# Kernel tuning notes

Measured on AMD Instinct MI355X. Metric: run time of the kernel, lower is better.

## Reference

```python
import jax, jax.numpy as jnp
import numpy as np

B, N, D, H, NC = 4, 32, 128, 8, 27
DK = D // H
DFF = 4 * D
L = NC * N


def layer_norm(x, g, b, eps=1e-5):
    mu = jnp.mean(x, -1, keepdims=True)
    var = jnp.var(x, -1, keepdims=True)
    return (x - mu) * jax.lax.rsqrt(var + eps) * g + b


def setup_inputs() -> dict:
    ks = jax.random.split(jax.random.key(0), 16)
    s = 1.0 / np.sqrt(D)
    return {
        'x': jax.random.normal(ks[0], (B, N, D), jnp.float32),
        'mask': jax.random.randint(ks[1], (B, 1, N), 0, 2, jnp.int32),
        'coords': jax.random.normal(ks[2], (B, NC, N, 3), jnp.float32),
        'Wp': jax.random.normal(ks[3], (3, D), jnp.float32) * 0.5,
        'bp': jnp.zeros((D,), jnp.float32),
        'Wq': jax.random.normal(ks[4], (D, D), jnp.float32) * s,
        'bq': jnp.zeros((D,), jnp.float32),
        'Wk': jax.random.normal(ks[5], (D, D), jnp.float32) * s,
        'bk': jnp.zeros((D,), jnp.float32),
        'Wv': jax.random.normal(ks[6], (D, D), jnp.float32) * s,
        'bv': jnp.zeros((D,), jnp.float32),
        'Wo': jax.random.normal(ks[7], (D, D), jnp.float32) * s,
        'bo': jnp.zeros((D,), jnp.float32),
        'g1': jnp.ones((D,), jnp.float32),
        'b1': jnp.zeros((D,), jnp.float32),
        'g2': jnp.ones((D,), jnp.float32),
        'b2': jnp.zeros((D,), jnp.float32),
        'W1': jax.random.normal(ks[8], (D, DFF), jnp.float32) * s,
        'bf1': jnp.zeros((DFF,), jnp.float32),
        'W2': jax.random.normal(ks[9], (DFF, D), jnp.float32) * (1.0 / np.sqrt(DFF)),
        'bf2': jnp.zeros((D,), jnp.float32),
    }


def reference(x, mask, coords, Wp, bp, Wq, bq, Wk, bk, Wv, bv, Wo, bo,
              g1, b1, g2, b2, W1, bf1, W2, bf2):
    mask_enh = jnp.tile(mask, (1, NC, 1)).reshape(B, 1, 1, L)

    def step(i):
        # position_encoding: x broadcast over 27 images + linear of coords relative to atom i
        ci = jax.lax.dynamic_slice_in_dim(coords, i, 1, axis=2)        # [B,NC,1,3]
        ar = x[:, None] + (coords - ci) @ Wp + bp                      # [B,NC,N,D]
        a = ar.reshape(B, L, D)
        hn = layer_norm(a, g1, b1)
        q = (hn @ Wq + bq).reshape(B, L, H, DK).transpose(0, 2, 1, 3)
        k = (hn @ Wk + bk).reshape(B, L, H, DK).transpose(0, 2, 1, 3)
        v = (hn @ Wv + bv).reshape(B, L, H, DK).transpose(0, 2, 1, 3)
        scores = jnp.einsum('bhqd,bhkd->bhqk', q, k) / np.sqrt(DK)     # [B,H,L,L]
        scores = jnp.where(mask_enh == 0, -1e9, scores)
        att = jnp.einsum('bhqk,bhkd->bhqd', jax.nn.softmax(scores, -1), v)
        att = att.transpose(0, 2, 1, 3).reshape(B, L, D) @ Wo + bo
        s = a + att  # SublayerConnection (dropout identity in eval)
        # original keeps only [b, image 0, atom i] of the [B,NC,N,D] reshape; flat index = i
        return jax.lax.dynamic_slice_in_dim(s, i, 1, axis=1)[:, 0]     # [B,D]

    rows = jax.lax.map(step, jnp.arange(N))                            # [N,B,D]
    y = rows.transpose(1, 0, 2)                                        # [B,N,D]
    hn2 = layer_norm(y, g2, b2)
    return y + (jax.nn.relu(hn2 @ W1 + bf1) @ W2 + bf2)
```

## Files before the change

### kernel.cpp

```cpp
#include <hip/hip_runtime.h>


#define B_ 4
#define N_ 32
#define D_ 128
#define H_ 8
#define NC_ 27
#define DFF_ 512
#define L_ (NC_*N_)

__device__ __forceinline__ float wred(float v){
  #pragma unroll
  for (int off = 32; off; off >>= 1) v += __shfl_xor(v, off);
  return v;
}

__global__ __launch_bounds__(1024) void k_fused(
    const float* __restrict__ x, const int* __restrict__ mask,
    const float* __restrict__ coords,
    const float* __restrict__ Wp, const float* __restrict__ bp,
    const float* __restrict__ Wq, const float* __restrict__ bq,
    const float* __restrict__ Wk, const float* __restrict__ bk,
    const float* __restrict__ Wv, const float* __restrict__ bv,
    const float* __restrict__ Wo, const float* __restrict__ bo,
    const float* __restrict__ g1, const float* __restrict__ b1,
    const float* __restrict__ g2, const float* __restrict__ b2,
    const float* __restrict__ W1, const float* __restrict__ bf1,
    const float* __restrict__ W2, const float* __restrict__ bfb2,
    float* __restrict__ out)
{
  __shared__ float is_s[L_];
  __shared__ float dc_s[3][L_];
  __shared__ float xg_s[N_][D_+1];
  __shared__ float zz_s[H_][D_+1];
  __shared__ float w_s[3][D_];
  __shared__ float wcg_s[3][D_];
  __shared__ float g1_s[D_], b1_s[D_], bp_s[D_], bq_s[D_], bk_s[D_];
  __shared__ float g2_s[D_], b2_s[D_], bv_s[D_], bo_s[D_], bfb2_s[D_];
  __shared__ float bf1_s[DFF_];
  __shared__ float q_s[D_], hn_s[D_], hn2_s[D_], att_s[D_], y_s[D_];
  __shared__ float qAxk_s[H_][N_];
  __shared__ float qGk_s[H_][3];
  __shared__ float S3_s[H_];
  __shared__ float varx_s[N_];
  __shared__ float dxp_s[N_][3];
  __shared__ int   mask_s[N_];
  __shared__ float cq_s[NC_][3];
  __shared__ float mwp_s[3], P6_s[6];
  __shared__ float pmax_s[H_][2];
  __shared__ float Tnp_s[H_][2][N_];
  __shared__ float Sp_s[H_][2], RDp_s[H_][2][3];
  __shared__ float f_s[DFF_];
  __shared__ float pf_s[4096];
  float4* pf4 = (float4*)pf_s;

  int bi = blockIdx.x;
  int b = bi >> 5, i = bi & 31;
  int tid = threadIdx.x, wave = tid >> 6, lane = tid & 63;
  int es = tid >> 5, d4 = tid & 31;
  int e0 = 2*lane, e1 = 2*lane+1;

  int r0 = wave*2, r1 = wave*2+1;
  float2 xA = *(const float2*)&x[(size_t)(b*N_+r0)*D_ + e0];
  float2 xB = *(const float2*)&x[(size_t)(b*N_+r1)*D_ + e0];
  float2 xI = {0.f, 0.f};
  if (wave == 0) xI = *(const float2*)&x[(size_t)bi*D_ + e0];
  float ck0=0.f, ck1=0.f, ck2=0.f;
  if (tid < L_){
    int c = tid >> 5, n = tid & 31;
    const float* ck = coords + ((size_t)(b*NC_+c)*N_ + n)*3;
    ck0 = ck[0]; ck1 = ck[1]; ck2 = ck[2];
  }
  float4 wq4[4];
  #pragma unroll
  for (int k=0;k<4;k++)
    wq4[k] = *(const float4*)(Wq + (size_t)(es*4+k)*D_ + d4*4);
  float4 wk4[4];
  {
    int h = tid>>7, e = tid&127;
    #pragma unroll
    for (int k=0;k<4;k++)
      wk4[k] = *(const float4*)(Wk + (size_t)e*D_ + h*16 + k*4);
  }
  if (tid < 384) w_s[tid>>7][tid&127] = Wp[tid];
  if      (tid < 128)  g1_s[tid]      = g1[tid];
  else if (tid < 256)  b1_s[tid-128]  = b1[tid-128];
  else if (tid < 384)  bp_s[tid-256]  = bp[tid-256];
  else if (tid < 512)  bq_s[tid-384]  = bq[tid-384];
  else if (tid < 640)  bk_s[tid-512]  = bk[tid-512];
  else if (tid < 768)  g2_s[tid-640]  = g2[tid-640];
  else if (tid < 896)  b2_s[tid-768]  = b2[tid-768];
  else                 bv_s[tid-896]  = bv[tid-896];
  if      (tid < 128)  bo_s[tid]      = bo[tid];
  else if (tid < 256)  bfb2_s[tid-128]= bfb2[tid-128];
  else if (tid < 768)  bf1_s[tid-256] = bf1[tid-256];
  else if (tid < 800)  mask_s[tid-768]= mask[b*N_ + (tid-768)];
  else if (tid < 881){
    int t = tid-800;
    cq_s[t/3][t%3] = coords[((size_t)(b*NC_ + t/3)*N_ + i)*3 + t%3];
  }
  __syncthreads();

  {
    float t0 = xA.x + bp_s[e0], t1 = xA.y + bp_s[e1];
    float mean = wred(t0+t1)*(1.f/D_);
    float h0 = t0-mean, h1 = t1-mean;
    xg_s[r0][e0] = h0*g1_s[e0];
    xg_s[r0][e1] = h1*g1_s[e1];
    float vv = h0*h0 + h1*h1;
    float d0 = h0*w_s[0][e0] + h1*w_s[0][e1];
    float d1 = h0*w_s[1][e0] + h1*w_s[1][e1];
    float d2 = h0*w_s[2][e0] + h1*w_s[2][e1];
    #pragma unroll
    for (int off=32; off; off>>=1){
      vv += __shfl_xor(vv,off); d0 += __shfl_xor(d0,off);
      d1 += __shfl_xor(d1,off); d2 += __shfl_xor(d2,off);
    }
    if (lane==0){ varx_s[r0]=vv*(1.f/D_);
      dxp_s[r0][0]=d0; dxp_s[r0][1]=d1; dxp_s[r0][2]=d2; }
    t0 = xB.x + bp_s[e0]; t1 = xB.y + bp_s[e1];
    mean = wred(t0+t1)*(1.f/D_);
    h0 = t0-mean; h1 = t1-mean;
    xg_s[r1][e0] = h0*g1_s[e0];
    xg_s[r1][e1] = h1*g1_s[e1];
    vv = h0*h0 + h1*h1;
    d0 = h0*w_s[0][e0] + h1*w_s[0][e1];
    d1 = h0*w_s[1][e0] + h1*w_s[1][e1];
    d2 = h0*w_s[2][e0] + h1*w_s[2][e1];
    #pragma unroll
    for (int off=32; off; off>>=1){
      vv += __shfl_xor(vv,off); d0 += __shfl_xor(d0,off);
      d1 += __shfl_xor(d1,off); d2 += __shfl_xor(d2,off);
    }
    if (lane==0){ varx_s[r1]=vv*(1.f/D_);
      dxp_s[r1][0]=d0; dxp_s[r1][1]=d1; dxp_s[r1][2]=d2; }
  }
  float dc0=0.f, dc1=0.f, dc2=0.f;
  if (tid < L_){
    int c = tid >> 5;
    dc0 = ck0 - cq_s[c][0]; dc1 = ck1 - cq_s[c][1]; dc2 = ck2 - cq_s[c][2];
    dc_s[0][tid]=dc0; dc_s[1][tid]=dc1; dc_s[2][tid]=dc2;
  }
  if (wave >= 8 && wave < 11){
    int j = wave - 8;
    float s = w_s[j][lane] + w_s[j][lane+64];
    s = wred(s);
    if (lane==0) mwp_s[j] = s*(1.f/D_);
  }
  if (wave >= 10){
    int idx = wave - 10;
    int ja = (idx>=3) + (idx>=5);
    int jb = idx - (idx>=3)*2 - (idx>=5);
    float s = w_s[ja][lane]*w_s[jb][lane] + w_s[ja][lane+64]*w_s[jb][lane+64];
    s = wred(s);
    if (lane==0) P6_s[idx] = s;
  }
  __syncthreads();

  if (tid < L_){
    int n = tid & 31;
    float m0 = mwp_s[0], m1 = mwp_s[1], m2 = mwp_s[2];
    float M00 = P6_s[0]-D_*m0*m0, M01 = P6_s[1]-D_*m0*m1;
    float M02 = P6_s[2]-D_*m0*m2, M11 = P6_s[3]-D_*m1*m1;
    float M12 = P6_s[4]-D_*m1*m2, M22 = P6_s[5]-D_*m2*m2;
    float quad = dc0*dc0*M00 + dc1*dc1*M11 + dc2*dc2*M22
               + 2.f*(dc0*dc1*M01 + dc0*dc2*M02 + dc1*dc2*M12);
    float lin  = dc0*dxp_s[n][0] + dc1*dxp_s[n][1] + dc2*dxp_s[n][2];
    float E = varx_s[n] + (quad + 2.f*lin)*(1.f/D_);
    is_s[tid] = rsqrtf(fmaxf(E, 0.f) + 1e-5f);
  }
  if (tid < 384){ int j=tid>>7, e=tid&127;
    wcg_s[j][e] = (w_s[j][e] - mwp_s[j])*g1_s[e]; }
  if (tid >= 896){ int e = tid-896;
    hn_s[e] = xg_s[i][e]*rsqrtf(varx_s[i]+1e-5f) + b1_s[e]; }
  __syncthreads();

  {
    float4 acc = {0.f,0.f,0.f,0.f};
    #pragma unroll
    for (int k=0;k<4;k++){
      float h = hn_s[es*4+k];
      acc.x += h*wq4[k].x; acc.y += h*wq4[k].y;
      acc.z += h*wq4[k].z; acc.w += h*wq4[k].w;
    }
    pf4[es*32 + d4] = acc;
  }
  __syncthreads();

  if (tid < D_){
    float a = bq_s[tid];
    #pragma unroll
    for (int s=0;s<32;s++) a += pf_s[s*D_+tid];
    q_s[tid] = a;
  }
  __syncthreads();

  {
    int h = tid>>7, e = tid&127;
    float s = 0.f;
    #pragma unroll
    for (int kq=0; kq<4; kq++){
      s += wk4[kq].x*q_s[h*16+kq*4+0] + wk4[kq].y*q_s[h*16+kq*4+1]
         + wk4[kq].z*q_s[h*16+kq*4+2] + wk4[kq].w*q_s[h*16+kq*4+3];
    }
    zz_s[h][e] = s;
  }
  __syncthreads();

  {
    int quarter = tid>>8, id = tid&255, h = id>>5, n = id&31;
    float s = 0.f;
    #pragma unroll 8
    for (int e = quarter*32; e < quarter*32+32; e++) s += xg_s[n][e]*zz_s[h][e];
    pf_s[quarter*256 + id] = s;
  }
  __syncthreads();

  if (tid < 256){
    qAxk_s[tid>>5][tid&31] = pf_s[tid] + pf_s[256+tid]
                           + pf_s[512+tid] + pf_s[768+tid];
  }
  if (wave >= 8){
    int h = wave - 8;
    float u0 = zz_s[h][lane], u1 = zz_s[h][lane+64];
    float s3 = b1_s[lane]*u0 + b1_s[lane+64]*u1;
    if (lane < 16) s3 += q_s[h*16+lane]*bk_s[h*16+lane];
    float qg0 = wcg_s[0][lane]*u0 + wcg_s[0][lane+64]*u1;
    float qg1 = wcg_s[1][lane]*u0 + wcg_s[1][lane+64]*u1;
    float qg2 = wcg_s[2][lane]*u0 + wcg_s[2][lane+64]*u1;
    #pragma unroll
    for (int off=32; off; off>>=1){
      s3  += __shfl_xor(s3,off);  qg0 += __shfl_xor(qg0,off);
      qg1 += __shfl_xor(qg1,off); qg2 += __shfl_xor(qg2,off);
    }
    if (lane==0){ S3_s[h]=s3; qGk_s[h][0]=qg0; qGk_s[h][1]=qg1; qGk_s[h][2]=qg2; }
  }
  __syncthreads();

  int h2 = wave>>1, sub = wave&1, n2 = lane&31, half2 = lane>>5;
  int q4 = sub*2 + half2, c0 = q4*7, c1 = (q4==3) ? NC_ : c0+7;
  float sc[7];
  {
    float qa = qAxk_s[h2][n2];
    float qg0 = qGk_s[h2][0], qg1 = qGk_s[h2][1], qg2 = qGk_s[h2][2];
    float s3 = S3_s[h2];
    bool mk = mask_s[n2] != 0;
    float M = -3.0e38f;
    #pragma unroll
    for (int t=0; t<7; t++){
      int c = c0+t;
      if (c < c1){
        int l = c*N_ + n2;
        float v = 0.25f*(is_s[l]*(qa + dc_s[0][l]*qg0 + dc_s[1][l]*qg1
                                     + dc_s[2][l]*qg2) + s3);
        sc[t] = mk ? v : -1e9f;
      } else sc[t] = -3.0e38f;
      M = fmaxf(M, sc[t]);
    }
    #pragma unroll
    for (int off=32; off; off>>=1) M = fmaxf(M, __shfl_xor(M, off));
    if (lane==0) pmax_s[h2][sub] = M;
  }
  __syncthreads();

  float4 wv4[4];
  #pragma unroll
  for (int k=0;k<4;k++)
    wv4[k] = *(const float4*)(Wv + (size_t)(es*4+k)*D_ + d4*4);
  {
    float M = fmaxf(pmax_s[h2][0], pmax_s[h2][1]);
    float S=0.f, Tn=0.f, rr0=0.f, rr1=0.f, rr2=0.f;
    #pragma unroll
    for (int t=0; t<7; t++){
      int c = c0+t;
      if (c < c1){
        int l = c*N_ + n2;
        float w_ = __expf(sc[t] - M);
        float tt = w_ * is_s[l];
        S += w_; Tn += tt;
        rr0 += tt*dc_s[0][l]; rr1 += tt*dc_s[1][l]; rr2 += tt*dc_s[2][l];
      }
    }
    float Tn2 = Tn + __shfl_xor(Tn, 32);
    if (lane < 32) Tnp_s[h2][sub][lane] = Tn2;
    #pragma unroll
    for (int off=32; off; off>>=1){
      S   += __shfl_xor(S,off);   rr0 += __shfl_xor(rr0,off);
      rr1 += __shfl_xor(rr1,off); rr2 += __shfl_xor(rr2,off);
    }
    if (lane==0){ Sp_s[h2][sub]=S;
      RDp_s[h2][sub][0]=rr0; RDp_s[h2][sub][1]=rr1; RDp_s[h2][sub][2]=rr2; }
  }
  __syncthreads();

  float4 wo4[4];
  #pragma unroll
  for (int k=0;k<4;k++)
    wo4[k] = *(const float4*)(Wo + (size_t)(es*4+k)*D_ + d4*4);
  {
    int h = tid>>7, e = tid&127;
    float rS = 1.f / fmaxf(Sp_s[h][0]+Sp_s[h][1], 1e-30f);
    float z = 0.f;
    #pragma unroll 8
    for (int n=0; n<N_; n++){
      float Tn = Tnp_s[h][0][n] + Tnp_s[h][1][n];
      z += Tn * xg_s[n][e];
    }
    float R0 = RDp_s[h][0][0]+RDp_s[h][1][0];
    float R1 = RDp_s[h][0][1]+RDp_s[h][1][1];
    float R2 = RDp_s[h][0][2]+RDp_s[h][1][2];
    z += R0*wcg_s[0][e] + R1*wcg_s[1][e] + R2*wcg_s[2][e];
    zz_s[h][e] = z*rS + b1_s[e];
  }
  __syncthreads();

  {
    int h = d4 >> 2;
    float4 acc = {0.f,0.f,0.f,0.f};
    #pragma unroll
    for (int k=0;k<4;k++){
      float zv = zz_s[h][es*4+k];
      acc.x += zv*wv4[k].x; acc.y += zv*wv4[k].y;
      acc.z += zv*wv4[k].z; acc.w += zv*wv4[k].w;
    }
    pf4[es*32 + d4] = acc;
  }
  __syncthreads();

  if (tid < D_){
    float a = bv_s[tid];
    #pragma unroll
    for (int s=0;s<32;s++) a += pf_s[s*D_+tid];
    att_s[tid] = a;
  }
  __syncthreads();

  int e8 = tid>>7, c4 = tid&127;
  float4 w1a[8];
  #pragma unroll
  for (int k=0;k<8;k++)
    w1a[k] = *(const float4*)(W1 + (size_t)(e8*16+k)*DFF_ + c4*4);
  {
    float4 acc = {0.f,0.f,0.f,0.f};
    #pragma unroll
    for (int k=0;k<4;k++){
      float av = att_s[es*4+k];
      acc.x += av*wo4[k].x; acc.y += av*wo4[k].y;
      acc.z += av*wo4[k].z; acc.w += av*wo4[k].w;
    }
    pf4[es*32 + d4] = acc;
  }
  __syncthreads();

  if (wave == 0){
    float y0 = xI.x + bp_s[e0] + bo_s[e0];
    float y1 = xI.y + bp_s[e1] + bo_s[e1];
    #pragma unroll
    for (int s=0;s<32;s++){
      float2 p = *(const float2*)&pf_s[s*D_ + e0];
      y0 += p.x; y1 += p.y;
    }
    y_s[e0] = y0; y_s[e1] = y1;
    float mean = wred(y0+y1)*(1.f/D_);
    float v0 = y0-mean, v1 = y1-mean;
    float var = wred(v0*v0+v1*v1)*(1.f/D_);
    float isd = rsqrtf(var + 1e-5f);
    hn2_s[e0] = v0*isd*g2_s[e0] + b2_s[e0];
    hn2_s[e1] = v1*isd*g2_s[e1] + b2_s[e1];
  }
  __syncthreads();

  int js = tid>>5;
  float4 w2a[8];
  {
    float4 w1b[8];
    #pragma unroll
    for (int k=0;k<8;k++)
      w1b[k] = *(const float4*)(W1 + (size_t)(e8*16+8+k)*DFF_ + c4*4);
    float4 acc = {0.f,0.f,0.f,0.f};
    #pragma unroll
    for (int k=0;k<8;k++){
      float h = hn2_s[e8*16+k];
      acc.x += h*w1a[k].x; acc.y += h*w1a[k].y;
      acc.z += h*w1a[k].z; acc.w += h*w1a[k].w;
    }
    #pragma unroll
    for (int k=0;k<8;k++){
      float h = hn2_s[e8*16+8+k];
      acc.x += h*w1b[k].x; acc.y += h*w1b[k].y;
      acc.z += h*w1b[k].z; acc.w += h*w1b[k].w;
    }
    #pragma unroll
    for (int k=0;k<8;k++)
      w2a[k] = *(const float4*)(W2 + (size_t)(js*16+k)*D_ + d4*4);
    pf4[e8*128 + c4] = acc;
  }
  __syncthreads();

  if (tid < DFF_){
    float a = bf1_s[tid];
    #pragma unroll
    for (int s=0;s<8;s++) a += pf_s[s*DFF_+tid];
    f_s[tid] = fmaxf(a, 0.f);
  }
  __syncthreads();

  {
    float4 w2b[8];
    #pragma unroll
    for (int k=0;k<8;k++)
      w2b[k] = *(const float4*)(W2 + (size_t)(js*16+8+k)*D_ + d4*4);
    float4 acc = {0.f,0.f,0.f,0.f};
    #pragma unroll
    for (int k=0;k<8;k++){
      float fv = f_s[js*16+k];
      acc.x += fv*w2a[k].x; acc.y += fv*w2a[k].y;
      acc.z += fv*w2a[k].z; acc.w += fv*w2a[k].w;
    }
    #pragma unroll
    for (int k=0;k<8;k++){
      float fv = f_s[js*16+8+k];
      acc.x += fv*w2b[k].x; acc.y += fv*w2b[k].y;
      acc.z += fv*w2b[k].z; acc.w += fv*w2b[k].w;
    }
    pf4[js*32 + d4] = acc;
  }
  __syncthreads();

  if (tid < D_){
    float a = y_s[tid] + bfb2_s[tid];
    #pragma unroll
    for (int s=0;s<32;s++) a += pf_s[s*D_+tid];
    out[(size_t)bi*D_ + tid] = a;
  }
}

extern "C" void kernel_launch(void* const* d_in, const int* in_sizes, int n_in,
                              void* d_out, int out_size, void* d_ws, size_t ws_size,
                              hipStream_t stream){
  const float* x      = (const float*)d_in[0];
  const int*   mask   = (const int*)  d_in[1];
  const float* coords = (const float*)d_in[2];
  const float* Wp     = (const float*)d_in[3];
  const float* bp     = (const float*)d_in[4];
  const float* Wq     = (const float*)d_in[5];
  const float* bq     = (const float*)d_in[6];
  const float* Wk     = (const float*)d_in[7];
  const float* bk     = (const float*)d_in[8];
  const float* Wv     = (const float*)d_in[9];
  const float* bv     = (const float*)d_in[10];
  const float* Wo     = (const float*)d_in[11];
  const float* bo     = (const float*)d_in[12];
  const float* g1     = (const float*)d_in[13];
  const float* b1     = (const float*)d_in[14];
  const float* g2     = (const float*)d_in[15];
  const float* b2     = (const float*)d_in[16];
  const float* W1     = (const float*)d_in[17];
  const float* bf1    = (const float*)d_in[18];
  const float* W2     = (const float*)d_in[19];
  const float* bfb2   = (const float*)d_in[20];

  k_fused<<<B_*N_, 1024, 0, stream>>>(x, mask, coords, Wp, bp, Wq, bq, Wk, bk,
                                      Wv, bv, Wo, bo, g1, b1, g2, b2,
                                      W1, bf1, W2, bfb2, (float*)d_out);
}
```

Measured before the change: 115.6 us.

## Remove block barriers by fusing LN row, split-max softmax, and full weight prefetch

The kernel now builds the normalized query row inside the first layer-norm pass, so the Q projection can run right after the first barrier and one barrier is gone. The softmax no longer syncs to share a global max. Each half-wave group uses its own local max, and the partial sums are rescaled by exp(M_i - M) when they are combined, which removes another barrier. All 16 rows of W1 and W2 are now loaded into registers early, rather than in two halves, so the load latency overlaps earlier work. The cost is higher register pressure on 1024-thread blocks, which could cause spills.

```diff
diff --git a/kernel.cpp b/kernel.cpp
--- a/kernel.cpp
+++ b/kernel.cpp
@@ -118,6 +118,11 @@
     }
     if (lane==0){ varx_s[r0]=vv*(1.f/D_);
       dxp_s[r0][0]=d0; dxp_s[r0][1]=d1; dxp_s[r0][2]=d2; }
+    if (r0 == i){
+      float isq = rsqrtf(vv*(1.f/D_)+1e-5f);
+      hn_s[e0] = h0*isq*g1_s[e0] + b1_s[e0];
+      hn_s[e1] = h1*isq*g1_s[e1] + b1_s[e1];
+    }
     t0 = xB.x + bp_s[e0]; t1 = xB.y + bp_s[e1];
     mean = wred(t0+t1)*(1.f/D_);
     h0 = t0-mean; h1 = t1-mean;
@@ -134,6 +139,11 @@
     }
     if (lane==0){ varx_s[r1]=vv*(1.f/D_);
       dxp_s[r1][0]=d0; dxp_s[r1][1]=d1; dxp_s[r1][2]=d2; }
+    if (r1 == i){
+      float isq = rsqrtf(vv*(1.f/D_)+1e-5f);
+      hn_s[e0] = h0*isq*g1_s[e0] + b1_s[e0];
+      hn_s[e1] = h1*isq*g1_s[e1] + b1_s[e1];
+    }
   }
   float dc0=0.f, dc1=0.f, dc2=0.f;
   if (tid < L_){
@@ -157,6 +167,16 @@
   }
   __syncthreads();
 
+  {
+    float4 acc = {0.f,0.f,0.f,0.f};
+    #pragma unroll
+    for (int k=0;k<4;k++){
+      float h = hn_s[es*4+k];
+      acc.x += h*wq4[k].x; acc.y += h*wq4[k].y;
+      acc.z += h*wq4[k].z; acc.w += h*wq4[k].w;
+    }
+    pf4[es*32 + d4] = acc;
+  }
   if (tid < L_){
     int n = tid & 31;
     float m0 = mwp_s[0], m1 = mwp_s[1], m2 = mwp_s[2];
@@ -171,20 +191,6 @@
   }
   if (tid < 384){ int j=tid>>7, e=tid&127;
     wcg_s[j][e] = (w_s[j][e] - mwp_s[j])*g1_s[e]; }
-  if (tid >= 896){ int e = tid-896;
-    hn_s[e] = xg_s[i][e]*rsqrtf(varx_s[i]+1e-5f) + b1_s[e]; }
-  __syncthreads();
-
-  {
-    float4 acc = {0.f,0.f,0.f,0.f};
-    #pragma unroll
-    for (int k=0;k<4;k++){
-      float h = hn_s[es*4+k];
-      acc.x += h*wq4[k].x; acc.y += h*wq4[k].y;
-      acc.z += h*wq4[k].z; acc.w += h*wq4[k].w;
-    }
-    pf4[es*32 + d4] = acc;
-  }
   __syncthreads();
 
   if (tid < D_){
@@ -239,12 +245,16 @@
 
   int h2 = wave>>1, sub = wave&1, n2 = lane&31, half2 = lane>>5;
   int q4 = sub*2 + half2, c0 = q4*7, c1 = (q4==3) ? NC_ : c0+7;
-  float sc[7];
+  float4 wv4[4];
+  #pragma unroll
+  for (int k=0;k<4;k++)
+    wv4[k] = *(const float4*)(Wv + (size_t)(es*4+k)*D_ + d4*4);
   {
     float qa = qAxk_s[h2][n2];
     float qg0 = qGk_s[h2][0], qg1 = qGk_s[h2][1], qg2 = qGk_s[h2][2];
     float s3 = S3_s[h2];
     bool mk = mask_s[n2] != 0;
+    float sc[7];
     float M = -3.0e38f;
     #pragma unroll
     for (int t=0; t<7; t++){
@@ -260,15 +270,6 @@
     #pragma unroll
     for (int off=32; off; off>>=1) M = fmaxf(M, __shfl_xor(M, off));
     if (lane==0) pmax_s[h2][sub] = M;
-  }
-  __syncthreads();
-
-  float4 wv4[4];
-  #pragma unroll
-  for (int k=0;k<4;k++)
-    wv4[k] = *(const float4*)(Wv + (size_t)(es*4+k)*D_ + d4*4);
-  {
-    float M = fmaxf(pmax_s[h2][0], pmax_s[h2][1]);
     float S=0.f, Tn=0.f, rr0=0.f, rr1=0.f, rr2=0.f;
     #pragma unroll
     for (int t=0; t<7; t++){
@@ -299,16 +300,20 @@
     wo4[k] = *(const float4*)(Wo + (size_t)(es*4+k)*D_ + d4*4);
   {
     int h = tid>>7, e = tid&127;
-    float rS = 1.f / fmaxf(Sp_s[h][0]+Sp_s[h][1], 1e-30f);
+    float M0 = pmax_s[h][0], M1 = pmax_s[h][1];
+    float Mx = fmaxf(M0, M1);
+    float f0 = __expf(M0-Mx), f1 = __expf(M1-Mx);
+    float S = Sp_s[h][0]*f0 + Sp_s[h][1]*f1;
+    float rS = 1.f / fmaxf(S, 1e-30f);
     float z = 0.f;
     #pragma unroll 8
     for (int n=0; n<N_; n++){
-      float Tn = Tnp_s[h][0][n] + Tnp_s[h][1][n];
+      float Tn = Tnp_s[h][0][n]*f0 + Tnp_s[h][1][n]*f1;
       z += Tn * xg_s[n][e];
     }
-    float R0 = RDp_s[h][0][0]+RDp_s[h][1][0];
-    float R1 = RDp_s[h][0][1]+RDp_s[h][1][1];
-    float R2 = RDp_s[h][0][2]+RDp_s[h][1][2];
+    float R0 = RDp_s[h][0][0]*f0 + RDp_s[h][1][0]*f1;
+    float R1 = RDp_s[h][0][1]*f0 + RDp_s[h][1][1]*f1;
+    float R2 = RDp_s[h][0][2]*f0 + RDp_s[h][1][2]*f1;
     z += R0*wcg_s[0][e] + R1*wcg_s[1][e] + R2*wcg_s[2][e];
     zz_s[h][e] = z*rS + b1_s[e];
   }
@@ -336,10 +341,10 @@
   __syncthreads();
 
   int e8 = tid>>7, c4 = tid&127;
-  float4 w1a[8];
-  #pragma unroll
-  for (int k=0;k<8;k++)
-    w1a[k] = *(const float4*)(W1 + (size_t)(e8*16+k)*DFF_ + c4*4);
+  float4 w14[16];
+  #pragma unroll
+  for (int k=0;k<16;k++)
+    w14[k] = *(const float4*)(W1 + (size_t)(e8*16+k)*DFF_ + c4*4);
   {
     float4 acc = {0.f,0.f,0.f,0.f};
     #pragma unroll
@@ -370,33 +375,23 @@
   }
   __syncthreads();
 
+  {
+    float4 acc = {0.f,0.f,0.f,0.f};
+    #pragma unroll
+    for (int k=0;k<16;k++){
+      float h = hn2_s[e8*16+k];
+      acc.x += h*w14[k].x; acc.y += h*w14[k].y;
+      acc.z += h*w14[k].z; acc.w += h*w14[k].w;
+    }
+    pf4[e8*128 + c4] = acc;
+  }
+  __syncthreads();
+
   int js = tid>>5;
-  float4 w2a[8];
-  {
-    float4 w1b[8];
-    #pragma unroll
-    for (int k=0;k<8;k++)
-      w1b[k] = *(const float4*)(W1 + (size_t)(e8*16+8+k)*DFF_ + c4*4);
-    float4 acc = {0.f,0.f,0.f,0.f};
-    #pragma unroll
-    for (int k=0;k<8;k++){
-      float h = hn2_s[e8*16+k];
-      acc.x += h*w1a[k].x; acc.y += h*w1a[k].y;
-      acc.z += h*w1a[k].z; acc.w += h*w1a[k].w;
-    }
-    #pragma unroll
-    for (int k=0;k<8;k++){
-      float h = hn2_s[e8*16+8+k];
-      acc.x += h*w1b[k].x; acc.y += h*w1b[k].y;
-      acc.z += h*w1b[k].z; acc.w += h*w1b[k].w;
-    }
-    #pragma unroll
-    for (int k=0;k<8;k++)
-      w2a[k] = *(const float4*)(W2 + (size_t)(js*16+k)*D_ + d4*4);
-    pf4[e8*128 + c4] = acc;
-  }
-  __syncthreads();
-
+  float4 w24[16];
+  #pragma unroll
+  for (int k=0;k<16;k++)
+    w24[k] = *(const float4*)(W2 + (size_t)(js*16+k)*D_ + d4*4);
   if (tid < DFF_){
     float a = bf1_s[tid];
     #pragma unroll
@@ -406,22 +401,12 @@
   __syncthreads();
 
   {
-    float4 w2b[8];
-    #pragma unroll
-    for (int k=0;k<8;k++)
-      w2b[k] = *(const float4*)(W2 + (size_t)(js*16+8+k)*D_ + d4*4);
     float4 acc = {0.f,0.f,0.f,0.f};
     #pragma unroll
-    for (int k=0;k<8;k++){
+    for (int k=0;k<16;k++){
       float fv = f_s[js*16+k];
-      acc.x += fv*w2a[k].x; acc.y += fv*w2a[k].y;
-      acc.z += fv*w2a[k].z; acc.w += fv*w2a[k].w;
-    }
-    #pragma unroll
-    for (int k=0;k<8;k++){
-      float fv = f_s[js*16+8+k];
-      acc.x += fv*w2b[k].x; acc.y += fv*w2b[k].y;
-      acc.z += fv*w2b[k].z; acc.w += fv*w2b[k].w;
+      acc.x += fv*w24[k].x; acc.y += fv*w24[k].y;
+      acc.z += fv*w24[k].z; acc.w += fv*w24[k].w;
     }
     pf4[js*32 + d4] = acc;
   }
```

Measured after the change: 115.4 us. No clear change (-0.2%).
